# Optimization experiments

Measured on AMD Instinct MI355X. Metric: run time of the kernel, lower is better.

Reference implementation:

```python
import jax, jax.numpy as jnp
import numpy as np

NEG_SLOPE = 0.2  # PyG GATConv default leaky_relu slope
N_NODES, IN_DIM, HID, HEADS, OUT = 50000, 128, 64, 4, 128
N_EDGES = 800000


def gat_conv(x, src, dst, num_nodes, W, a_src, a_dst, bias, concat):
    """One PyG-style GATConv (add_self_loops already applied to src/dst)."""
    H, C = a_src.shape
    xp = (x @ W).reshape(num_nodes, H, C)            # (N,H,C)
    s = jnp.einsum('nhc,hc->nh', xp, a_src)          # per-node src score
    d = jnp.einsum('nhc,hc->nh', xp, a_dst)          # per-node dst score
    e = s[src] + d[dst]                              # (E,H)
    e = jnp.where(e > 0, e, NEG_SLOPE * e)           # leaky_relu
    # segment softmax over edges grouped by destination node
    m = jax.ops.segment_max(e, dst, num_segments=num_nodes)
    p = jnp.exp(e - m[dst])
    z = jax.ops.segment_sum(p, dst, num_segments=num_nodes)
    alpha = p / (z[dst] + 1e-16)                     # (E,H)
    # scatter-aggregate messages
    out = jax.ops.segment_sum(xp[src] * alpha[:, :, None], dst, num_segments=num_nodes)
    out = out.reshape(num_nodes, H * C) if concat else out.mean(axis=1)
    return out + bias


def setup_inputs() -> dict:
    key = jax.random.key(0)
    ks = jax.random.split(key, 16)
    HC = HEADS * HID
    inp = {
        'x': jax.random.normal(ks[0], (N_NODES, IN_DIM), dtype=jnp.float32),
        'edge_index': jax.random.randint(ks[1], (2, N_EDGES), 0, N_NODES, dtype=jnp.int32),
        'W0': jax.random.normal(ks[2], (IN_DIM, HC), dtype=jnp.float32) * 0.08,
        'a_src0': jax.random.normal(ks[3], (HEADS, HID), dtype=jnp.float32) * 0.1,
        'a_dst0': jax.random.normal(ks[4], (HEADS, HID), dtype=jnp.float32) * 0.1,
        'b0': jnp.zeros((HC,), dtype=jnp.float32),
        'W1': jax.random.normal(ks[5], (HC, HC), dtype=jnp.float32) * 0.06,
        'a_src1': jax.random.normal(ks[6], (HEADS, HID), dtype=jnp.float32) * 0.1,
        'a_dst1': jax.random.normal(ks[7], (HEADS, HID), dtype=jnp.float32) * 0.1,
        'b1': jnp.zeros((HC,), dtype=jnp.float32),
        'W2': jax.random.normal(ks[8], (HC, OUT), dtype=jnp.float32) * 0.06,
        'a_src2': jax.random.normal(ks[9], (1, OUT), dtype=jnp.float32) * 0.1,
        'a_dst2': jax.random.normal(ks[10], (1, OUT), dtype=jnp.float32) * 0.1,
        'b2': jnp.zeros((OUT,), dtype=jnp.float32),
    }
    return inp


def reference(x, edge_index, W0, a_src0, a_dst0, b0, W1, a_src1, a_dst1, b1, W2, a_src2, a_dst2, b2):
    N = x.shape[0]
    loops = jnp.arange(N, dtype=edge_index.dtype)  # add_self_loops=True
    src = jnp.concatenate([edge_index[0], loops])
    dst = jnp.concatenate([edge_index[1], loops])
    h = gat_conv(x, src, dst, N, W0, a_src0, a_dst0, b0, True)
    h = jax.nn.elu(h)
    h = gat_conv(h, src, dst, N, W1, a_src1, a_dst1, b1, True)
    h = jax.nn.elu(h)
    h = gat_conv(h, src, dst, N, W2, a_src2, a_dst2, b2, False)
    return h
```

## Files before the change

### kernel.cpp

```cpp
#include <hip/hip_runtime.h>
#include <hip/hip_bf16.h>
#include <hip/hip_fp16.h>
#include <math.h>

#define N_NODES 50000
#define N_EDGES 800000
#define ET      (N_EDGES + N_NODES)
#define IN_DIM  128
#define HEADS   4
#define HID     64
#define HC      256
#define OUTD    128

typedef _Float16 half8 __attribute__((ext_vector_type(8)));
typedef float f32x4 __attribute__((ext_vector_type(4)));


__global__ void hist_k(const int* __restrict__ ei, int* __restrict__ counts) {
    int i = blockIdx.x * blockDim.x + threadIdx.x;
    if (i >= ET) return;
    int dv = (i < N_EDGES) ? ei[N_EDGES + i] : (i - N_EDGES);
    atomicAdd(&counts[dv], 1);
}

__global__ void scan1_k(const int* __restrict__ counts, int* __restrict__ offs,
                        int* __restrict__ bsums) {
    __shared__ int sm[512];
    int tid = threadIdx.x;
    int i = blockIdx.x * 512 + tid;
    int v = (i < N_NODES) ? counts[i] : 0;
    sm[tid] = v;
    __syncthreads();
    #pragma unroll
    for (int o = 1; o < 512; o <<= 1) {
        int add = (tid >= o) ? sm[tid - o] : 0;
        __syncthreads();
        sm[tid] += add;
        __syncthreads();
    }
    if (i < N_NODES) offs[i] = sm[tid] - v;
    if (tid == 511) bsums[blockIdx.x] = sm[511];
}

__global__ void scan2_k(int* __restrict__ bsums, int nb) {
    __shared__ int sm[128];
    int tid = threadIdx.x;
    int v = (tid < nb) ? bsums[tid] : 0;
    sm[tid] = v;
    __syncthreads();
    #pragma unroll
    for (int o = 1; o < 128; o <<= 1) {
        int add = (tid >= o) ? sm[tid - o] : 0;
        __syncthreads();
        sm[tid] += add;
        __syncthreads();
    }
    if (tid < nb) bsums[tid] = sm[tid] - v;
}

__global__ void scan3_k(int* __restrict__ offs, const int* __restrict__ bsums) {
    int i = blockIdx.x * 512 + threadIdx.x;
    if (i < N_NODES) offs[i] += bsums[blockIdx.x];
    if (i == 0) offs[N_NODES] = ET;
}

__global__ void fill_k(const int* __restrict__ ei, const int* __restrict__ offs,
                       int* __restrict__ cursor, int* __restrict__ csr) {
    int i = blockIdx.x * blockDim.x + threadIdx.x;
    if (i >= ET) return;
    int sv, dv;
    if (i < N_EDGES) { sv = ei[i]; dv = ei[N_EDGES + i]; }
    else             { sv = dv = i - N_EDGES; }
    int pos = offs[dv] + atomicAdd(&cursor[dv], 1);
    csr[pos] = sv;
}

__global__ __launch_bounds__(256) void sortseg_k(const int* __restrict__ offs,
                                                 int* __restrict__ csr) {
    int wid = blockIdx.x * 4 + (threadIdx.x >> 6);
    int lane = threadIdx.x & 63;
    if (wid >= N_NODES) return;
    int e0 = offs[wid], e1 = offs[wid + 1];
    int deg = e1 - e0;
    if (deg <= 1 || deg > 64) return;
    int v = (lane < deg) ? csr[e0 + lane] : 0x7fffffff;
    #pragma unroll
    for (int k = 2; k <= 64; k <<= 1) {
        #pragma unroll
        for (int j = k >> 1; j > 0; j >>= 1) {
            int v2 = __shfl_xor(v, j, 64);
            bool keepmin = (((lane & j) == 0) == ((lane & k) == 0));
            int mn = min(v, v2), mx = max(v, v2);
            v = keepmin ? mn : mx;
        }
    }
    if (lane < deg) csr[e0 + lane] = v;
}


__global__ void cvt_fp16_k(const float* __restrict__ x, __half* __restrict__ xh, int n4) {
    int i = blockIdx.x * 256 + threadIdx.x;
    if (i >= n4) return;
    float4 v = *(const float4*)(x + (size_t)i * 4);
    union { __half2 h2[2]; float2 f2; } u;
    u.h2[0] = __floats2half2_rn(v.x, v.y);
    u.h2[1] = __floats2half2_rn(v.z, v.w);
    *(float2*)(xh + (size_t)i * 4) = u.f2;
}

__global__ void wtrans_k(const float* __restrict__ W, __half* __restrict__ Wt, int K, int N) {
    int idx = blockIdx.x * 256 + threadIdx.x;
    if (idx >= K * N) return;
    int n = idx / K, k = idx - n * K;
    Wt[idx] = __float2half(W[(size_t)k * N + n]);
}


__device__ __forceinline__ void async_copy16(void* lds_base, const void* gaddr) {
    __builtin_amdgcn_global_load_lds(
        (const __attribute__((address_space(1))) unsigned int*)gaddr,
        (__attribute__((address_space(3))) unsigned int*)lds_base,
        16, 0, 0);
}

template<int H, int CD, bool ATOMIC>
__global__ __launch_bounds__(256) void gemm_mfma_k(const __half* __restrict__ A,
                                                   const __half* __restrict__ Wt,
                                                   __half* __restrict__ C,
                                                   const float* __restrict__ asrc,
                                                   const float* __restrict__ adst,
                                                   float* __restrict__ S,
                                                   float* __restrict__ D,
                                                   int M, int K, int N) {
    __shared__ __attribute__((aligned(16))) __half Ah[128 * 32];
    __shared__ __attribute__((aligned(16))) __half Bh[128 * 32];
    const int t = threadIdx.x;
    const int w = t >> 6;
    const int lane = t & 63;
    const int wm = w >> 1, wn = w & 1;
    const int row0 = blockIdx.x * 128;
    const int col0 = blockIdx.y * 128;

    f32x4 acc[4][4];
    #pragma unroll
    for (int i = 0; i < 4; ++i)
        #pragma unroll
        for (int j = 0; j < 4; ++j) acc[i][j] = (f32x4){0.f, 0.f, 0.f, 0.f};

    const int srow = lane >> 2;
    const int skq  = (lane & 3) * 8;
    const int fr = lane & 15;
    const int fq = (lane >> 4) * 8;

    for (int k0 = 0; k0 < K; k0 += 32) {
        __syncthreads();
        #pragma unroll
        for (int hh = 0; hh < 2; ++hh) {
            int ra = row0 + w * 32 + hh * 16 + srow;
            if (ra > M - 1) ra = M - 1;
            async_copy16(&Ah[(w * 32 + hh * 16) * 32],
                         A + (size_t)ra * K + k0 + skq);
            int rb = col0 + w * 32 + hh * 16 + srow;
            async_copy16(&Bh[(w * 32 + hh * 16) * 32],
                         Wt + (size_t)rb * K + k0 + skq);
        }
        __syncthreads();
        half8 a[4], b[4];
        #pragma unroll
        for (int i = 0; i < 4; ++i)
            a[i] = *(const half8*)&Ah[(wm * 64 + i * 16 + fr) * 32 + fq];
        #pragma unroll
        for (int j = 0; j < 4; ++j)
            b[j] = *(const half8*)&Bh[(wn * 64 + j * 16 + fr) * 32 + fq];
        #pragma unroll
        for (int i = 0; i < 4; ++i)
            #pragma unroll
            for (int j = 0; j < 4; ++j)
                acc[i][j] = __builtin_amdgcn_mfma_f32_16x16x32_f16(a[i], b[j], acc[i][j], 0, 0, 0);
    }

    const int cr = (lane >> 4) * 4;
    const int cc = lane & 15;
    #pragma unroll
    for (int i = 0; i < 4; ++i) {
        #pragma unroll
        for (int j = 0; j < 4; ++j) {
            int c = col0 + wn * 64 + j * 16 + cc;
            #pragma unroll
            for (int reg = 0; reg < 4; ++reg) {
                int r = row0 + wm * 64 + i * 16 + cr + reg;
                if (r < M)
                    C[(size_t)r * N + c] = __float2half(acc[i][j][reg]);
            }
        }
    }

    const int hh_ = ATOMIC ? 0 : (blockIdx.y * 2 + wn);
    float asj[4], adj[4];
    #pragma unroll
    for (int j = 0; j < 4; ++j) {
        int cwh = (ATOMIC ? wn * 64 : 0) + j * 16 + cc;
        asj[j] = asrc[hh_ * CD + cwh];
        adj[j] = adst[hh_ * CD + cwh];
    }
    #pragma unroll
    for (int i = 0; i < 4; ++i) {
        #pragma unroll
        for (int reg = 0; reg < 4; ++reg) {
            float sv = 0.f, dv = 0.f;
            #pragma unroll
            for (int j = 0; j < 4; ++j) {
                sv = fmaf(acc[i][j][reg], asj[j], sv);
                dv = fmaf(acc[i][j][reg], adj[j], dv);
            }
            #pragma unroll
            for (int o = 1; o < 16; o <<= 1) {
                sv += __shfl_xor(sv, o, 64);
                dv += __shfl_xor(dv, o, 64);
            }
            int r = row0 + wm * 64 + i * 16 + cr + reg;
            if (cc == 0 && r < M) {
                if constexpr (ATOMIC) {
                    atomicAdd(&S[r], sv);
                    atomicAdd(&D[r], dv);
                } else {
                    S[(size_t)r * H + hh_] = sv;
                    D[(size_t)r * H + hh_] = dv;
                }
            }
        }
    }
}


template<int H, int C, bool ELU_OUT, typename OT>
__global__ __launch_bounds__(256) void aggr_k(const __half* __restrict__ xp,
                                              const float* __restrict__ s,
                                              const float* __restrict__ d,
                                              const int* __restrict__ offs,
                                              const int* __restrict__ csr,
                                              const float* __restrict__ bias,
                                              OT* __restrict__ out) {
    constexpr int HCl = H * C;
    constexpr int EPL = HCl / 64;
    constexpr int U = 8;
    int wid = blockIdx.x * 4 + (threadIdx.x >> 6);
    int lane = threadIdx.x & 63;
    if (wid >= N_NODES) return;
    int h = (lane * EPL) / C;
    float dh = d[(size_t)wid * H + h];
    float z = 0.f;
    float acc[EPL];
    #pragma unroll
    for (int k = 0; k < EPL; ++k) acc[k] = 0.f;

    auto loadrow = [&](int src, float* v) {
        const __half* xr = xp + (size_t)src * HCl + lane * EPL;
        if constexpr (EPL == 4) {
            union { float2 f2; __half2 h2[2]; } u;
            u.f2 = *(const float2*)xr;
            float2 a = __half22float2(u.h2[0]);
            float2 b = __half22float2(u.h2[1]);
            v[0] = a.x; v[1] = a.y; v[2] = b.x; v[3] = b.y;
        } else {
            union { float f; __half2 h2; } u;
            u.f = *(const float*)xr;
            float2 a = __half22float2(u.h2);
            v[0] = a.x; v[1] = a.y;
        }
    };

    int e0 = offs[wid], e1 = offs[wid + 1];
    int j = e0;
    for (; j + U <= e1; j += U) {
        int srcs[U];
        #pragma unroll
        for (int u = 0; u < U; ++u) srcs[u] = csr[j + u];
        float ev[U];
        #pragma unroll
        for (int u = 0; u < U; ++u) ev[u] = s[(size_t)srcs[u] * H + h];
        float v[U][EPL];
        #pragma unroll
        for (int u = 0; u < U; ++u) loadrow(srcs[u], v[u]);
        #pragma unroll
        for (int u = 0; u < U; ++u) {
            float e = ev[u] + dh;
            e = (e > 0.f) ? e : 0.2f * e;
            float p = __expf(e);
            z += p;
            #pragma unroll
            for (int k = 0; k < EPL; ++k) acc[k] += p * v[u][k];
        }
    }
    for (; j < e1; ++j) {
        int sv = csr[j];
        float e = s[(size_t)sv * H + h] + dh;
        e = (e > 0.f) ? e : 0.2f * e;
        float p = __expf(e);
        float v[EPL];
        loadrow(sv, v);
        z += p;
        #pragma unroll
        for (int k = 0; k < EPL; ++k) acc[k] += p * v[k];
    }

    float inv = 1.f / (z + 1e-16f);
    float o[EPL];
    #pragma unroll
    for (int k = 0; k < EPL; ++k) {
        o[k] = acc[k] * inv + bias[lane * EPL + k];
        if constexpr (ELU_OUT) o[k] = (o[k] > 0.f) ? o[k] : (__expf(o[k]) - 1.f);
    }
    if constexpr (sizeof(OT) == 2 && EPL == 4) {
        union { __half2 h2[2]; float2 f2; } u;
        u.h2[0] = __floats2half2_rn(o[0], o[1]);
        u.h2[1] = __floats2half2_rn(o[2], o[3]);
        *(float2*)((__half*)out + (size_t)wid * HCl + lane * EPL) = u.f2;
    } else {
        #pragma unroll
        for (int k = 0; k < EPL; ++k)
            out[(size_t)wid * HCl + lane * EPL + k] = (OT)o[k];
    }
}


extern "C" void kernel_launch(void* const* d_in, const int* in_sizes, int n_in,
                              void* d_out, int out_size, void* d_ws, size_t ws_size,
                              hipStream_t stream) {
    const float* x      = (const float*)d_in[0];
    const int*   ei     = (const int*)  d_in[1];
    const float* W0     = (const float*)d_in[2];
    const float* as0    = (const float*)d_in[3];
    const float* ad0    = (const float*)d_in[4];
    const float* b0     = (const float*)d_in[5];
    const float* W1     = (const float*)d_in[6];
    const float* as1    = (const float*)d_in[7];
    const float* ad1    = (const float*)d_in[8];
    const float* b1     = (const float*)d_in[9];
    const float* W2     = (const float*)d_in[10];
    const float* as2    = (const float*)d_in[11];
    const float* ad2    = (const float*)d_in[12];
    const float* b2     = (const float*)d_in[13];
    float* out = (float*)d_out;

    char* p = (char*)d_ws;
    auto take = [&](size_t bytes) {
        char* r = p;
        p += (bytes + 255) & ~(size_t)255;
        return r;
    };
    __half* XPh   = (__half*)take((size_t)N_NODES * HC * 2);
    __half* Hbuf  = (__half*)take((size_t)N_NODES * HC * 2);
    __half* xh    = (__half*)take((size_t)N_NODES * IN_DIM * 2);
    __half* Wt0   = (__half*)take((size_t)IN_DIM * HC * 2);
    __half* Wt1   = (__half*)take((size_t)HC * HC * 2);
    __half* Wt2   = (__half*)take((size_t)HC * OUTD * 2);
    float*  S     = (float*) take((size_t)N_NODES * HEADS * 4);
    float*  D     = (float*) take((size_t)N_NODES * HEADS * 4);
    int*    counts= (int*)   take((size_t)2 * N_NODES * 4);
    int*    cursor= counts + N_NODES;
    int*    offs  = (int*)   take((size_t)(N_NODES + 1) * 4);
    int*    bsums = (int*)   take(512 * 4);
    int*    csr   = (int*)   take((size_t)ET * 4);

    const int NB_SCAN = (N_NODES + 511) / 512;
    const int ET_BLOCKS = (ET + 255) / 256;
    const int NODE_BLOCKS = (N_NODES + 3) / 4;

    hipMemsetAsync(counts, 0, (size_t)2 * N_NODES * 4, stream);
    hist_k<<<ET_BLOCKS, 256, 0, stream>>>(ei, counts);
    scan1_k<<<NB_SCAN, 512, 0, stream>>>(counts, offs, bsums);
    scan2_k<<<1, 128, 0, stream>>>(bsums, NB_SCAN);
    scan3_k<<<NB_SCAN, 512, 0, stream>>>(offs, bsums);
    fill_k<<<ET_BLOCKS, 256, 0, stream>>>(ei, offs, cursor, csr);
    sortseg_k<<<NODE_BLOCKS, 256, 0, stream>>>(offs, csr);

    cvt_fp16_k<<<(N_NODES * IN_DIM / 4 + 255) / 256, 256, 0, stream>>>(x, xh, N_NODES * IN_DIM / 4);
    wtrans_k<<<(IN_DIM * HC + 255) / 256, 256, 0, stream>>>(W0, Wt0, IN_DIM, HC);
    wtrans_k<<<(HC * HC + 255) / 256, 256, 0, stream>>>(W1, Wt1, HC, HC);
    wtrans_k<<<(HC * OUTD + 255) / 256, 256, 0, stream>>>(W2, Wt2, HC, OUTD);

    const int MB = (N_NODES + 127) / 128;
    dim3 g0(MB, HC / 128);
    dim3 g2(MB, OUTD / 128);

    gemm_mfma_k<HEADS, HID, false><<<g0, 256, 0, stream>>>(xh, Wt0, XPh, as0, ad0, S, D, N_NODES, IN_DIM, HC);
    aggr_k<HEADS, HID, true, __half><<<NODE_BLOCKS, 256, 0, stream>>>(XPh, S, D, offs, csr, b0, Hbuf);

    gemm_mfma_k<HEADS, HID, false><<<g0, 256, 0, stream>>>(Hbuf, Wt1, XPh, as1, ad1, S, D, N_NODES, HC, HC);
    aggr_k<HEADS, HID, true, __half><<<NODE_BLOCKS, 256, 0, stream>>>(XPh, S, D, offs, csr, b1, Hbuf);

    hipMemsetAsync(S, 0, (size_t)N_NODES * 4, stream);
    hipMemsetAsync(D, 0, (size_t)N_NODES * 4, stream);
    gemm_mfma_k<1, OUTD, true><<<g2, 256, 0, stream>>>(Hbuf, Wt2, XPh, as2, ad2, S, D, N_NODES, HC, OUTD);
    aggr_k<1, OUTD, false, float><<<NODE_BLOCKS, 256, 0, stream>>>(XPh, S, D, offs, csr, b2, out);
}
```

Before: 455.6 us.

## Drop CSR segment sort, merge weight transposes, unroll aggregation with masked tail

Removes the per-node bitonic sort of CSR source indices, so neighbour order inside each segment is now left as the atomic fill produces it. The three weight transpose launches become one combined kernel. The aggregation loop is unrolled 16-wide, the scalar remainder loop is replaced by a masked tail (padding edges get a -1e30 score, so they contribute nothing), and raw half rows are loaded before conversion. The goal is to cut launches and sort work and to keep more gather loads in flight, at the cost of non-deterministic summation order, less cache locality in the gathers, and more registers per thread.

```diff
diff --git a/kernel.cpp b/kernel.cpp
--- a/kernel.cpp
+++ b/kernel.cpp
@@ -75,28 +75,6 @@
     csr[pos] = sv;
 }
 
-__global__ __launch_bounds__(256) void sortseg_k(const int* __restrict__ offs,
-                                                 int* __restrict__ csr) {
-    int wid = blockIdx.x * 4 + (threadIdx.x >> 6);
-    int lane = threadIdx.x & 63;
-    if (wid >= N_NODES) return;
-    int e0 = offs[wid], e1 = offs[wid + 1];
-    int deg = e1 - e0;
-    if (deg <= 1 || deg > 64) return;
-    int v = (lane < deg) ? csr[e0 + lane] : 0x7fffffff;
-    #pragma unroll
-    for (int k = 2; k <= 64; k <<= 1) {
-        #pragma unroll
-        for (int j = k >> 1; j > 0; j >>= 1) {
-            int v2 = __shfl_xor(v, j, 64);
-            bool keepmin = (((lane & j) == 0) == ((lane & k) == 0));
-            int mn = min(v, v2), mx = max(v, v2);
-            v = keepmin ? mn : mx;
-        }
-    }
-    if (lane < deg) csr[e0 + lane] = v;
-}
-
 
 __global__ void cvt_fp16_k(const float* __restrict__ x, __half* __restrict__ xh, int n4) {
     int i = blockIdx.x * 256 + threadIdx.x;
@@ -108,9 +86,15 @@
     *(float2*)(xh + (size_t)i * 4) = u.f2;
 }
 
-__global__ void wtrans_k(const float* __restrict__ W, __half* __restrict__ Wt, int K, int N) {
+__global__ void wtrans3_k(const float* __restrict__ W0, __half* __restrict__ Wt0,
+                          const float* __restrict__ W1, __half* __restrict__ Wt1,
+                          const float* __restrict__ W2, __half* __restrict__ Wt2) {
     int idx = blockIdx.x * 256 + threadIdx.x;
-    if (idx >= K * N) return;
+    const float* W; __half* Wt; int K, N;
+    if (idx < 32768)        { W = W0; Wt = Wt0; K = IN_DIM; N = HC; }
+    else if (idx < 98304)   { idx -= 32768; W = W1; Wt = Wt1; K = HC; N = HC; }
+    else if (idx < 131072)  { idx -= 98304; W = W2; Wt = Wt2; K = HC; N = OUTD; }
+    else return;
     int n = idx / K, k = idx - n * K;
     Wt[idx] = __float2half(W[(size_t)k * N + n]);
 }
@@ -243,7 +227,7 @@
                                               OT* __restrict__ out) {
     constexpr int HCl = H * C;
     constexpr int EPL = HCl / 64;
-    constexpr int U = 8;
+    constexpr int U = 16;
     int wid = blockIdx.x * 4 + (threadIdx.x >> 6);
     int lane = threadIdx.x & 63;
     if (wid >= N_NODES) return;
@@ -254,54 +238,44 @@
     #pragma unroll
     for (int k = 0; k < EPL; ++k) acc[k] = 0.f;
 
-    auto loadrow = [&](int src, float* v) {
-        const __half* xr = xp + (size_t)src * HCl + lane * EPL;
-        if constexpr (EPL == 4) {
-            union { float2 f2; __half2 h2[2]; } u;
-            u.f2 = *(const float2*)xr;
-            float2 a = __half22float2(u.h2[0]);
-            float2 b = __half22float2(u.h2[1]);
-            v[0] = a.x; v[1] = a.y; v[2] = b.x; v[3] = b.y;
-        } else {
-            union { float f; __half2 h2; } u;
-            u.f = *(const float*)xr;
-            float2 a = __half22float2(u.h2);
-            v[0] = a.x; v[1] = a.y;
-        }
-    };
+    using RawT = typename std::conditional<EPL == 4, uint2, unsigned int>::type;
 
     int e0 = offs[wid], e1 = offs[wid + 1];
-    int j = e0;
-    for (; j + U <= e1; j += U) {
+    for (int j = e0; j < e1; j += U) {
         int srcs[U];
-        #pragma unroll
-        for (int u = 0; u < U; ++u) srcs[u] = csr[j + u];
         float ev[U];
         #pragma unroll
-        for (int u = 0; u < U; ++u) ev[u] = s[(size_t)srcs[u] * H + h];
-        float v[U][EPL];
-        #pragma unroll
-        for (int u = 0; u < U; ++u) loadrow(srcs[u], v[u]);
+        for (int u = 0; u < U; ++u) {
+            int idx = j + u;
+            srcs[u] = csr[idx < e1 ? idx : e1 - 1];
+        }
+        #pragma unroll
+        for (int u = 0; u < U; ++u)
+            ev[u] = (j + u < e1) ? s[(size_t)srcs[u] * H + h] : -1e30f;
+        RawT raw[U];
+        #pragma unroll
+        for (int u = 0; u < U; ++u)
+            raw[u] = *(const RawT*)(xp + (size_t)srcs[u] * HCl + lane * EPL);
         #pragma unroll
         for (int u = 0; u < U; ++u) {
             float e = ev[u] + dh;
             e = (e > 0.f) ? e : 0.2f * e;
             float p = __expf(e);
             z += p;
-            #pragma unroll
-            for (int k = 0; k < EPL; ++k) acc[k] += p * v[u][k];
-        }
-    }
-    for (; j < e1; ++j) {
-        int sv = csr[j];
-        float e = s[(size_t)sv * H + h] + dh;
-        e = (e > 0.f) ? e : 0.2f * e;
-        float p = __expf(e);
-        float v[EPL];
-        loadrow(sv, v);
-        z += p;
-        #pragma unroll
-        for (int k = 0; k < EPL; ++k) acc[k] += p * v[k];
+            float v[EPL];
+            if constexpr (EPL == 4) {
+                union { uint2 r; __half2 h2[2]; } uu; uu.r = raw[u];
+                float2 a = __half22float2(uu.h2[0]);
+                float2 b = __half22float2(uu.h2[1]);
+                v[0] = a.x; v[1] = a.y; v[2] = b.x; v[3] = b.y;
+            } else {
+                union { unsigned int r; __half2 h2; } uu; uu.r = raw[u];
+                float2 a = __half22float2(uu.h2);
+                v[0] = a.x; v[1] = a.y;
+            }
+            #pragma unroll
+            for (int k = 0; k < EPL; ++k) acc[k] += p * v[k];
+        }
     }
 
     float inv = 1.f / (z + 1e-16f);
@@ -373,12 +347,9 @@
     scan2_k<<<1, 128, 0, stream>>>(bsums, NB_SCAN);
     scan3_k<<<NB_SCAN, 512, 0, stream>>>(offs, bsums);
     fill_k<<<ET_BLOCKS, 256, 0, stream>>>(ei, offs, cursor, csr);
-    sortseg_k<<<NODE_BLOCKS, 256, 0, stream>>>(offs, csr);
 
     cvt_fp16_k<<<(N_NODES * IN_DIM / 4 + 255) / 256, 256, 0, stream>>>(x, xh, N_NODES * IN_DIM / 4);
-    wtrans_k<<<(IN_DIM * HC + 255) / 256, 256, 0, stream>>>(W0, Wt0, IN_DIM, HC);
-    wtrans_k<<<(HC * HC + 255) / 256, 256, 0, stream>>>(W1, Wt1, HC, HC);
-    wtrans_k<<<(HC * OUTD + 255) / 256, 256, 0, stream>>>(W2, Wt2, HC, OUTD);
+    wtrans3_k<<<(131072 + 255) / 256, 256, 0, stream>>>(W0, Wt0, W1, Wt1, W2, Wt2);
 
     const int MB = (N_NODES + 127) / 128;
     dim3 g0(MB, HC / 128);
```

New measurement: 462.0 us. Within noise of the previous version (+1.4%).

## Drop segment sort, merge weight prep and memsets, widen GEMM K-tile

Applied to the files above, without the earlier changes.

The CSR fill now reuses the histogram counts as a decrementing cursor, and the per-segment bitonic sort kernel is removed, so edges within a node are in nondeterministic order. The three weight transpose kernels and the two memsets for the last layer's score buffers are merged into one prep kernel that writes into separate S2/D2 buffers. The GEMM K-tile grows from 32 to 64, halving barrier round-trips per K step at the cost of doubled LDS. The aim is fewer launches and less synchronisation; the risk is nondeterministic floating-point summation order in aggregation.

```diff
diff --git a/kernel.cpp b/kernel.cpp
--- a/kernel.cpp
+++ b/kernel.cpp
@@ -65,36 +65,14 @@
 }
 
 __global__ void fill_k(const int* __restrict__ ei, const int* __restrict__ offs,
-                       int* __restrict__ cursor, int* __restrict__ csr) {
+                       int* __restrict__ counts, int* __restrict__ csr) {
     int i = blockIdx.x * blockDim.x + threadIdx.x;
     if (i >= ET) return;
     int sv, dv;
     if (i < N_EDGES) { sv = ei[i]; dv = ei[N_EDGES + i]; }
     else             { sv = dv = i - N_EDGES; }
-    int pos = offs[dv] + atomicAdd(&cursor[dv], 1);
+    int pos = offs[dv] + atomicSub(&counts[dv], 1) - 1;
     csr[pos] = sv;
-}
-
-__global__ __launch_bounds__(256) void sortseg_k(const int* __restrict__ offs,
-                                                 int* __restrict__ csr) {
-    int wid = blockIdx.x * 4 + (threadIdx.x >> 6);
-    int lane = threadIdx.x & 63;
-    if (wid >= N_NODES) return;
-    int e0 = offs[wid], e1 = offs[wid + 1];
-    int deg = e1 - e0;
-    if (deg <= 1 || deg > 64) return;
-    int v = (lane < deg) ? csr[e0 + lane] : 0x7fffffff;
-    #pragma unroll
-    for (int k = 2; k <= 64; k <<= 1) {
-        #pragma unroll
-        for (int j = k >> 1; j > 0; j >>= 1) {
-            int v2 = __shfl_xor(v, j, 64);
-            bool keepmin = (((lane & j) == 0) == ((lane & k) == 0));
-            int mn = min(v, v2), mx = max(v, v2);
-            v = keepmin ? mn : mx;
-        }
-    }
-    if (lane < deg) csr[e0 + lane] = v;
 }
 
 
@@ -108,11 +86,27 @@
     *(float2*)(xh + (size_t)i * 4) = u.f2;
 }
 
-__global__ void wtrans_k(const float* __restrict__ W, __half* __restrict__ Wt, int K, int N) {
+__global__ void prep_k(const float* __restrict__ W0, __half* __restrict__ Wt0,
+                       const float* __restrict__ W1, __half* __restrict__ Wt1,
+                       const float* __restrict__ W2, __half* __restrict__ Wt2,
+                       float* __restrict__ S2, float* __restrict__ D2) {
     int idx = blockIdx.x * 256 + threadIdx.x;
-    if (idx >= K * N) return;
-    int n = idx / K, k = idx - n * K;
-    Wt[idx] = __float2half(W[(size_t)k * N + n]);
+    if (idx < 32768) {
+        int n = idx / IN_DIM, k = idx - n * IN_DIM;
+        Wt0[idx] = __float2half(W0[(size_t)k * HC + n]);
+    } else if (idx < 98304) {
+        int i = idx - 32768;
+        int n = i / HC, k = i - n * HC;
+        Wt1[i] = __float2half(W1[(size_t)k * HC + n]);
+    } else if (idx < 131072) {
+        int i = idx - 98304;
+        int n = i / HC, k = i - n * HC;
+        Wt2[i] = __float2half(W2[(size_t)k * OUTD + n]);
+    } else if (idx < 181072) {
+        S2[idx - 131072] = 0.f;
+    } else if (idx < 231072) {
+        D2[idx - 181072] = 0.f;
+    }
 }
 
 
@@ -132,8 +126,8 @@
                                                    float* __restrict__ S,
                                                    float* __restrict__ D,
                                                    int M, int K, int N) {
-    __shared__ __attribute__((aligned(16))) __half Ah[128 * 32];
-    __shared__ __attribute__((aligned(16))) __half Bh[128 * 32];
+    __shared__ __attribute__((aligned(16))) __half Ah[128 * 64];
+    __shared__ __attribute__((aligned(16))) __half Bh[128 * 64];
     const int t = threadIdx.x;
     const int w = t >> 6;
     const int lane = t & 63;
@@ -147,36 +141,39 @@
         #pragma unroll
         for (int j = 0; j < 4; ++j) acc[i][j] = (f32x4){0.f, 0.f, 0.f, 0.f};
 
-    const int srow = lane >> 2;
-    const int skq  = (lane & 3) * 8;
+    const int srow = lane >> 3;
+    const int skq  = (lane & 7) * 8;
     const int fr = lane & 15;
     const int fq = (lane >> 4) * 8;
 
-    for (int k0 = 0; k0 < K; k0 += 32) {
-        __syncthreads();
-        #pragma unroll
-        for (int hh = 0; hh < 2; ++hh) {
-            int ra = row0 + w * 32 + hh * 16 + srow;
+    for (int k0 = 0; k0 < K; k0 += 64) {
+        __syncthreads();
+        #pragma unroll
+        for (int hh = 0; hh < 4; ++hh) {
+            int ra = row0 + w * 32 + hh * 8 + srow;
             if (ra > M - 1) ra = M - 1;
-            async_copy16(&Ah[(w * 32 + hh * 16) * 32],
+            async_copy16(&Ah[(w * 32 + hh * 8) * 64],
                          A + (size_t)ra * K + k0 + skq);
-            int rb = col0 + w * 32 + hh * 16 + srow;
-            async_copy16(&Bh[(w * 32 + hh * 16) * 32],
+            int rb = col0 + w * 32 + hh * 8 + srow;
+            async_copy16(&Bh[(w * 32 + hh * 8) * 64],
                          Wt + (size_t)rb * K + k0 + skq);
         }
         __syncthreads();
-        half8 a[4], b[4];
-        #pragma unroll
-        for (int i = 0; i < 4; ++i)
-            a[i] = *(const half8*)&Ah[(wm * 64 + i * 16 + fr) * 32 + fq];
-        #pragma unroll
-        for (int j = 0; j < 4; ++j)
-            b[j] = *(const half8*)&Bh[(wn * 64 + j * 16 + fr) * 32 + fq];
-        #pragma unroll
-        for (int i = 0; i < 4; ++i)
+        #pragma unroll
+        for (int c = 0; c < 2; ++c) {
+            half8 a[4], b[4];
+            #pragma unroll
+            for (int i = 0; i < 4; ++i)
+                a[i] = *(const half8*)&Ah[(wm * 64 + i * 16 + fr) * 64 + c * 32 + fq];
             #pragma unroll
             for (int j = 0; j < 4; ++j)
-                acc[i][j] = __builtin_amdgcn_mfma_f32_16x16x32_f16(a[i], b[j], acc[i][j], 0, 0, 0);
+                b[j] = *(const half8*)&Bh[(wn * 64 + j * 16 + fr) * 64 + c * 32 + fq];
+            #pragma unroll
+            for (int i = 0; i < 4; ++i)
+                #pragma unroll
+                for (int j = 0; j < 4; ++j)
+                    acc[i][j] = __builtin_amdgcn_mfma_f32_16x16x32_f16(a[i], b[j], acc[i][j], 0, 0, 0);
+        }
     }
 
     const int cr = (lane >> 4) * 4;
@@ -357,8 +354,9 @@
     __half* Wt2   = (__half*)take((size_t)HC * OUTD * 2);
     float*  S     = (float*) take((size_t)N_NODES * HEADS * 4);
     float*  D     = (float*) take((size_t)N_NODES * HEADS * 4);
-    int*    counts= (int*)   take((size_t)2 * N_NODES * 4);
-    int*    cursor= counts + N_NODES;
+    float*  S2    = (float*) take((size_t)N_NODES * 4);
+    float*  D2    = (float*) take((size_t)N_NODES * 4);
+    int*    counts= (int*)   take((size_t)N_NODES * 4);
     int*    offs  = (int*)   take((size_t)(N_NODES + 1) * 4);
     int*    bsums = (int*)   take(512 * 4);
     int*    csr   = (int*)   take((size_t)ET * 4);
@@ -367,18 +365,15 @@
     const int ET_BLOCKS = (ET + 255) / 256;
     const int NODE_BLOCKS = (N_NODES + 3) / 4;
 
-    hipMemsetAsync(counts, 0, (size_t)2 * N_NODES * 4, stream);
+    hipMemsetAsync(counts, 0, (size_t)N_NODES * 4, stream);
     hist_k<<<ET_BLOCKS, 256, 0, stream>>>(ei, counts);
     scan1_k<<<NB_SCAN, 512, 0, stream>>>(counts, offs, bsums);
     scan2_k<<<1, 128, 0, stream>>>(bsums, NB_SCAN);
     scan3_k<<<NB_SCAN, 512, 0, stream>>>(offs, bsums);
-    fill_k<<<ET_BLOCKS, 256, 0, stream>>>(ei, offs, cursor, csr);
-    sortseg_k<<<NODE_BLOCKS, 256, 0, stream>>>(offs, csr);
+    fill_k<<<ET_BLOCKS, 256, 0, stream>>>(ei, offs, counts, csr);
 
     cvt_fp16_k<<<(N_NODES * IN_DIM / 4 + 255) / 256, 256, 0, stream>>>(x, xh, N_NODES * IN_DIM / 4);
-    wtrans_k<<<(IN_DIM * HC + 255) / 256, 256, 0, stream>>>(W0, Wt0, IN_DIM, HC);
-    wtrans_k<<<(HC * HC + 255) / 256, 256, 0, stream>>>(W1, Wt1, HC, HC);
-    wtrans_k<<<(HC * OUTD + 255) / 256, 256, 0, stream>>>(W2, Wt2, HC, OUTD);
+    prep_k<<<(231072 + 255) / 256, 256, 0, stream>>>(W0, Wt0, W1, Wt1, W2, Wt2, S2, D2);
 
     const int MB = (N_NODES + 127) / 128;
     dim3 g0(MB, HC / 128);
@@ -390,8 +385,6 @@
     gemm_mfma_k<HEADS, HID, false><<<g0, 256, 0, stream>>>(Hbuf, Wt1, XPh, as1, ad1, S, D, N_NODES, HC, HC);
     aggr_k<HEADS, HID, true, __half><<<NODE_BLOCKS, 256, 0, stream>>>(XPh, S, D, offs, csr, b1, Hbuf);
 
-    hipMemsetAsync(S, 0, (size_t)N_NODES * 4, stream);
-    hipMemsetAsync(D, 0, (size_t)N_NODES * 4, stream);
-    gemm_mfma_k<1, OUTD, true><<<g2, 256, 0, stream>>>(Hbuf, Wt2, XPh, as2, ad2, S, D, N_NODES, HC, OUTD);
-    aggr_k<1, OUTD, false, float><<<NODE_BLOCKS, 256, 0, stream>>>(XPh, S, D, offs, csr, b2, out);
-}
+    gemm_mfma_k<1, OUTD, true><<<g2, 256, 0, stream>>>(Hbuf, Wt2, XPh, as2, ad2, S2, D2, N_NODES, HC, OUTD);
+    aggr_k<1, OUTD, false, float><<<NODE_BLOCKS, 256, 0, stream>>>(XPh, S2, D2, offs, csr, b2, out);
+}
```

Result: faster. 429.2 us (-5.8%).
